# Optimization experiments

Measured on AMD Instinct MI355X. Metric: run time of the kernel, lower is better.

Reference implementation:

```python
import jax, jax.numpy as jnp
import numpy as np
import math

B, S, E, H = 2, 2048, 1024, 8
Dh = E // H  # 128


def setup_inputs() -> dict:
    key = jax.random.key(0)
    ks = jax.random.split(key, 9)
    g = lambda k, shp: jax.random.normal(k, shp, jnp.float32) * 0.02
    return {
        "inputs": jax.random.normal(ks[0], (B, S, E), jnp.float32),
        "ln_gamma": jnp.ones((E,), jnp.float32),
        "ln_beta": jnp.zeros((E,), jnp.float32),
        "Wq": g(ks[1], (Dh, Dh)), "bq": jnp.zeros((Dh,), jnp.float32),
        "Wk": g(ks[2], (Dh, Dh)), "bk": jnp.zeros((Dh,), jnp.float32),
        "Wv": g(ks[3], (Dh, Dh)), "bv": jnp.zeros((Dh,), jnp.float32),
        "Wp": g(ks[4], (Dh, Dh)),  # pos_proj has no bias
        "u_bias": g(ks[5], (H, Dh)),
        "v_bias": g(ks[6], (H, Dh)),
        "Wo": g(ks[7], (E, E)), "bo": jnp.zeros((E,), jnp.float32),
    }


def _pos_encoding(s, e):
    # sinusoidal PE, interleaved sin/cos as in the torch module
    pos = jnp.arange(s, dtype=jnp.float32)[:, None]
    div = jnp.exp(jnp.arange(0, e, 2, dtype=jnp.float32) * (-math.log(10000.0) / e))
    pe = jnp.zeros((s, e), jnp.float32)
    pe = pe.at[:, 0::2].set(jnp.sin(pos * div))
    pe = pe.at[:, 1::2].set(jnp.cos(pos * div))
    return pe


def _rel_shift(ps):
    # Transformer-XL relative shift: pad a zero column, reshape, drop first row
    b, h, s1, s2 = ps.shape
    padded = jnp.pad(ps, ((0, 0), (0, 0), (0, 0), (1, 0)))
    return padded.reshape(b, h, s2 + 1, s1)[:, :, 1:, :].reshape(b, h, s1, s2)


def _forward(inputs, ln_gamma, ln_beta, Wq, bq, Wk, bk, Wv, bv, Wp, u_bias, v_bias, Wo, bo):
    b, s, e = inputs.shape
    # LayerNorm (biased variance, eps=1e-5 like nn.LayerNorm)
    mu = inputs.mean(-1, keepdims=True)
    var = inputs.var(-1, keepdims=True)
    xn = (inputs - mu) / jnp.sqrt(var + 1e-5) * ln_gamma + ln_beta

    xh = xn.reshape(b, s, H, Dh)              # split heads before per-head Dh x Dh projections
    q = xh @ Wq + bq                           # (b, s, H, Dh)
    k = xh @ Wk + bk
    v = xh @ Wv + bv

    pe = _pos_encoding(s, e).reshape(s, H, Dh)  # same for every batch element
    p = pe @ Wp                                 # (s, H, Dh)

    content = jnp.einsum('bqhd,bkhd->bhqk', q + u_bias, k)
    pos_score = jnp.einsum('bqhd,khd->bhqk', q + v_bias, p)
    pos_score = _rel_shift(pos_score)
    score = (content + pos_score) / jnp.sqrt(jnp.float32(e))  # note: scales by sqrt(embed_dim), faithful to source

    attn = jax.nn.softmax(score, axis=-1)
    ctx = jnp.einsum('bhqk,bkhd->bqhd', attn, v).reshape(b, s, e)
    # dropout is identity at inference
    return ctx @ Wo + bo


def reference(inputs, ln_gamma, ln_beta, Wq, bq, Wk, bk, Wv, bv, Wp, u_bias, v_bias, Wo, bo):
    return _forward(inputs, ln_gamma, ln_beta, Wq, bq, Wk, bk, Wv, bv, Wp, u_bias, v_bias, Wo, bo)
```

## Files before the change

kernel.cpp:

```cpp
#include <hip/hip_runtime.h>
#include <hip/hip_bf16.h>

#define SDIM 2048
#define EDIM 1024

typedef __attribute__((ext_vector_type(8))) short bf16x8;
typedef __attribute__((ext_vector_type(4))) short bf16x4;
typedef __attribute__((ext_vector_type(4))) float f32x4;
typedef __hip_bfloat16 bf16;

#define MFMA(a, b, c) __builtin_amdgcn_mfma_f32_16x16x32_bf16((a), (b), (c), 0, 0, 0)

#define GLDS16(g, l)                                                      \
  __builtin_amdgcn_global_load_lds(                                       \
      (const __attribute__((address_space(1))) unsigned int*)(g),         \
      (__attribute__((address_space(3))) unsigned int*)(l), 16, 0, 0)

__device__ __forceinline__ bf16x8 ld8(const bf16* p) {
  return *(const bf16x8*)p;
}
__device__ __forceinline__ float b2f(short s) {
  union { float f; unsigned u; } v; v.u = ((unsigned)(unsigned short)s) << 16; return v.f;
}

__device__ __forceinline__ void wcast_body(const float* __restrict__ w, bf16* __restrict__ wt,
                                           int blk, int R, int C) {
  __shared__ float tile[32][33];
  int cb = C >> 5;
  int br = blk / cb, bc = blk % cb;
  int r0 = br << 5, c0 = bc << 5;
  int tr = threadIdx.x >> 5, tc = threadIdx.x & 31;
#pragma unroll
  for (int i = 0; i < 32; i += 8)
    tile[tr + i][tc] = w[(size_t)(r0 + tr + i) * C + c0 + tc];
  __syncthreads();
#pragma unroll
  for (int i = 0; i < 32; i += 8)
    wt[(size_t)(c0 + tr + i) * R + r0 + tc] = __float2bfloat16(tile[tc][tr + i]);
}

__global__ __launch_bounds__(256) void wcast_all(const float* __restrict__ wo, const float* __restrict__ w0,
                                                 const float* __restrict__ w1, const float* __restrict__ w2,
                                                 const float* __restrict__ w3, bf16* __restrict__ oo,
                                                 bf16* __restrict__ o0, bf16* __restrict__ o1,
                                                 bf16* __restrict__ o2, bf16* __restrict__ o3) {
  int blk = blockIdx.x;
  if (blk < 1024) {
    wcast_body(wo, oo, blk, 1024, 1024);
  } else {
    int which = (blk - 1024) >> 4;
    const float* w = which == 0 ? w0 : which == 1 ? w1 : which == 2 ? w2 : w3;
    bf16* o = which == 0 ? o0 : which == 1 ? o1 : which == 2 ? o2 : o3;
    wcast_body(w, o, (blk - 1024) & 15, 128, 128);
  }
}

__global__ __launch_bounds__(256) void ln_kernel(const float* __restrict__ x, const float* __restrict__ g,
                                                 const float* __restrict__ be, bf16* __restrict__ xn) {
  int tok = blockIdx.x;
  const float4 v = ((const float4*)(x + (size_t)tok * EDIM))[threadIdx.x];
  float s = v.x + v.y + v.z + v.w;
  float s2 = v.x * v.x + v.y * v.y + v.z * v.z + v.w * v.w;
#pragma unroll
  for (int o = 1; o < 64; o <<= 1) { s += __shfl_xor(s, o); s2 += __shfl_xor(s2, o); }
  __shared__ float ls[8];
  if ((threadIdx.x & 63) == 0) { ls[threadIdx.x >> 6] = s; ls[4 + (threadIdx.x >> 6)] = s2; }
  __syncthreads();
  s = ls[0] + ls[1] + ls[2] + ls[3];
  s2 = ls[4] + ls[5] + ls[6] + ls[7];
  float mu = s * (1.0f / EDIM);
  float rstd = rsqrtf(s2 * (1.0f / EDIM) - mu * mu + 1e-5f);
  int c = threadIdx.x * 4;
  const float4 gv = ((const float4*)g)[threadIdx.x];
  const float4 bv = ((const float4*)be)[threadIdx.x];
  bf16* o = xn + (size_t)tok * EDIM + c;
  o[0] = __float2bfloat16((v.x - mu) * rstd * gv.x + bv.x);
  o[1] = __float2bfloat16((v.y - mu) * rstd * gv.y + bv.y);
  o[2] = __float2bfloat16((v.z - mu) * rstd * gv.z + bv.z);
  o[3] = __float2bfloat16((v.w - mu) * rstd * gv.w + bv.w);
}

__global__ __launch_bounds__(256) void pe_kernel(bf16* __restrict__ pe) {
  int s = blockIdx.x;
  for (int i = threadIdx.x; i < EDIM / 2; i += 256) {
    float div = __expf((float)(2 * i) * (-9.210340371976184f / (float)EDIM));
    float a = (float)s * div;
    float sv, cv;
    sincosf(a, &sv, &cv);
    pe[(size_t)s * EDIM + 2 * i] = __float2bfloat16(sv);
    pe[(size_t)s * EDIM + 2 * i + 1] = __float2bfloat16(cv);
  }
}

template <int MODE>
__device__ __forceinline__ void proj_body(const bf16* __restrict__ A, const bf16* __restrict__ WT,
                                          const float* __restrict__ bias, const float* __restrict__ ubias,
                                          const float* __restrict__ vbias, bf16* __restrict__ out0,
                                          bf16* __restrict__ out1, int blk, bf16* tl) {
  const int row0 = blk * 128;
  const int lane = threadIdx.x & 63, wid = threadIdx.x >> 6;
  const int wr = (wid >> 1) * 64, wc = (wid & 1) * 64;
  const int lg = lane >> 4, lr = lane & 15;
  f32x4 acc[4][4] = {};
#pragma unroll
  for (int kf = 0; kf < 4; ++kf) {
    const int k0 = kf * 32 + lg * 8;
    bf16x8 a[4], b[4];
#pragma unroll
    for (int m = 0; m < 4; ++m) a[m] = ld8(A + (size_t)(row0 + wr + m * 16 + lr) * 128 + k0);
#pragma unroll
    for (int n = 0; n < 4; ++n) b[n] = ld8(WT + (size_t)(wc + n * 16 + lr) * 128 + k0);
#pragma unroll
    for (int m = 0; m < 4; ++m)
#pragma unroll
      for (int n = 0; n < 4; ++n) acc[m][n] = MFMA(a[m], b[n], acc[m][n]);
  }
  if constexpr (MODE == 2) {
#pragma unroll
    for (int m = 0; m < 4; ++m)
#pragma unroll
      for (int n = 0; n < 4; ++n) {
        int col = wc + n * 16 + lr;
#pragma unroll
        for (int r = 0; r < 4; ++r) {
          int lrow = wr + m * 16 + lg * 4 + r;
          tl[col * 132 + lrow] = __float2bfloat16(acc[m][n][r] + bias[col]);
        }
      }
    __syncthreads();
    int tok0 = row0 >> 3;
    int b = tok0 >> 11, s0 = tok0 & 2047;
#pragma unroll
    for (int i = 0; i < 4; ++i) {
      int pair = threadIdx.x + 256 * i;
      int h = pair >> 7, d = pair & 127;
      bf16 tmp[16];
#pragma unroll
      for (int j = 0; j < 16; ++j) tmp[j] = tl[d * 132 + j * 8 + h];
      size_t o = ((size_t)((b * 8 + h) * 128 + d)) * SDIM + s0;
      *(bf16x8*)(out0 + o) = *(bf16x8*)(&tmp[0]);
      *(bf16x8*)(out0 + o + 8) = *(bf16x8*)(&tmp[8]);
    }
  } else {
#pragma unroll
    for (int m = 0; m < 4; ++m)
#pragma unroll
      for (int n = 0; n < 4; ++n) {
        int col = wc + n * 16 + lr;
#pragma unroll
        for (int r = 0; r < 4; ++r) {
          int row = row0 + wr + m * 16 + lg * 4 + r;
          float val = acc[m][n][r];
          if constexpr (MODE == 0) {
            int h = row & 7, tok = row >> 3;
            int b = tok >> 11, s = tok & 2047;
            size_t o = ((size_t)((b * 8 + h) * SDIM + s)) * 128 + col;
            val += bias[col];
            out0[o] = __float2bfloat16((val + ubias[h * 128 + col]) * 0.03125f);
            out1[o] = __float2bfloat16((val + vbias[h * 128 + col]) * 0.03125f);
          } else if constexpr (MODE == 1) {
            int h = row & 7, tok = row >> 3;
            int b = tok >> 11, s = tok & 2047;
            out0[((size_t)((b * 8 + h) * SDIM + s)) * 128 + col] = __float2bfloat16(val + bias[col]);
          } else {
            int h = row & 7, s = row >> 3;
            out0[((size_t)(h * SDIM + s)) * 128 + col] = __float2bfloat16(val);
          }
        }
      }
  }
}

__global__ __launch_bounds__(256) void proj_all(const bf16* __restrict__ xn, const bf16* __restrict__ peb,
                                                const bf16* __restrict__ wqt, const bf16* __restrict__ wkt,
                                                const bf16* __restrict__ wvt, const bf16* __restrict__ wpt,
                                                const float* __restrict__ bq, const float* __restrict__ bk,
                                                const float* __restrict__ bv, const float* __restrict__ ub,
                                                const float* __restrict__ vbias, bf16* __restrict__ qub,
                                                bf16* __restrict__ qvb, bf16* __restrict__ kbb,
                                                bf16* __restrict__ vtb, bf16* __restrict__ pb) {
  __shared__ bf16 tl[128 * 132];
  int blk = blockIdx.x;
  if (blk < 256) proj_body<0>(xn, wqt, bq, ub, vbias, qub, qvb, blk, tl);
  else if (blk < 512) proj_body<1>(xn, wkt, bk, nullptr, nullptr, kbb, nullptr, blk - 256, tl);
  else if (blk < 768) proj_body<2>(xn, wvt, bv, nullptr, nullptr, vtb, nullptr, blk - 512, tl);
  else proj_body<3>(peb, wpt, nullptr, nullptr, nullptr, pb, nullptr, blk - 768, tl);
}

__global__ __launch_bounds__(256) void ps_kernel(const bf16* __restrict__ qv, const bf16* __restrict__ p,
                                                 bf16* __restrict__ ps) {
  const int bh = blockIdx.x & 15;
  const int t = blockIdx.x >> 4;
  const int q0 = (t >> 4) * 128, j0 = (t & 15) * 128;
  const int h = bh & 7;
  const bf16* Aq = qv + (size_t)bh * SDIM * 128;
  const bf16* Ph = p + (size_t)h * SDIM * 128;
  const int lane = threadIdx.x & 63, wid = threadIdx.x >> 6;
  const int wr = (wid >> 1) * 64, wc = (wid & 1) * 64;
  const int lg = lane >> 4, lr = lane & 15;
  f32x4 acc[4][4] = {};
#pragma unroll
  for (int kf = 0; kf < 4; ++kf) {
    const int k0 = kf * 32 + lg * 8;
    bf16x8 a[4], b[4];
#pragma unroll
    for (int m = 0; m < 4; ++m) a[m] = ld8(Aq + (size_t)(q0 + wr + m * 16 + lr) * 128 + k0);
#pragma unroll
    for (int n = 0; n < 4; ++n) b[n] = ld8(Ph + (size_t)(j0 + wc + n * 16 + lr) * 128 + k0);
#pragma unroll
    for (int m = 0; m < 4; ++m)
#pragma unroll
      for (int n = 0; n < 4; ++n) acc[m][n] = MFMA(a[m], b[n], acc[m][n]);
  }
  __shared__ bf16 tl[128 * 136];
#pragma unroll
  for (int m = 0; m < 4; ++m)
#pragma unroll
    for (int n = 0; n < 4; ++n) {
      int jl = wc + n * 16 + lr;
#pragma unroll
      for (int r = 0; r < 4; ++r) {
        int ql = wr + m * 16 + lg * 4 + r;
        tl[ql * 136 + jl] = __float2bfloat16(acc[m][n][r]);
      }
    }
  __syncthreads();
  bf16* po = ps + (size_t)bh * SDIM * SDIM + (size_t)q0 * SDIM + j0;
#pragma unroll
  for (int i = 0; i < 8; ++i) {
    int id = threadIdx.x + 256 * i;
    int row = id >> 4, seg = id & 15;
    bf16x8 v = *(const bf16x8*)(tl + row * 136 + seg * 8);
    *(bf16x8*)(po + (size_t)row * SDIM + seg * 8) = v;
  }
}

__global__ __launch_bounds__(512) void attn_kernel(const bf16* __restrict__ qu, const bf16* __restrict__ kb,
                                                   const bf16* __restrict__ vt, const bf16* __restrict__ ps,
                                                   bf16* __restrict__ ctx) {
  const int bh = blockIdx.x & 15, qblk = blockIdx.x >> 4;
  const int b = bh >> 3, h = bh & 7;
  const int lane = threadIdx.x & 63, wid = threadIdx.x >> 6;
  const int lg = lane >> 4, lr = lane & 15;
  const int q0 = qblk * 128 + wid * 16;
  const bf16* Kp = kb + (size_t)bh * SDIM * 128;
  const bf16* Vp = vt + (size_t)bh * 128 * SDIM;

  const bf16* psbh = ps + (size_t)bh * SDIM * SDIM;
  const int Q = q0 + lr;
  const bf16* pA = psbh + (size_t)(Q + 1) * (SDIM - 1);
  const bf16* pB = psbh + (size_t)(Q + 1) * SDIM - Q - 2;
  const int padA = (int)(((unsigned)(Q + 1) * (SDIM - 1)) & 3);
  const int padB = (int)(((unsigned)(Q + 1) * SDIM - Q - 2) & 3);

  __shared__ bf16 kl[2][64 * 128];
  __shared__ bf16 vl[2][128 * 64];
  __shared__ bf16 pl[8][16 * 72];
  bf16* plw = &pl[wid][0];

  const int krow_l = lane >> 4, kc16 = lane & 15;
  const int vrow_l = lane >> 3, vc8 = lane & 7;

  auto stageK = [&](int kt, int buf) {
#pragma unroll
    for (int i = 0; i < 2; ++i) {
      int rb = wid * 8 + i * 4;
      int row = rb + krow_l;
      GLDS16(Kp + (size_t)(kt + row) * 128 + ((kc16 ^ (row & 7)) << 3), &kl[buf][rb * 128]);
    }
  };
  auto stageV = [&](int kt, int buf) {
#pragma unroll
    for (int i = 0; i < 2; ++i) {
      int rb = wid * 16 + i * 8;
      int d = rb + vrow_l;
      GLDS16(Vp + (size_t)d * SDIM + kt + ((vc8 ^ (d & 7)) << 3), &vl[buf][rb * 64]);
    }
  };

  bf16x8 qfr[4];
#pragma unroll
  for (int kf = 0; kf < 4; ++kf)
    qfr[kf] = ld8(qu + (size_t)bh * SDIM * 128 + (size_t)(q0 + lr) * 128 + kf * 32 + lg * 8);

  f32x4 cacc[8] = {};
  float rsum = 0.f;

  unsigned long long wlo[4], whi[4];
  auto psload = [&](int kt) {
#pragma unroll
    for (int nf = 0; nf < 4; ++nf) {
      const int K0 = kt + nf * 16 + lg * 4;
      const bool a_ = (K0 + 3 <= Q);
      const bf16* wp = a_ ? (pA + K0 - padA) : (pB + K0 - padB);
      wlo[nf] = *(const unsigned long long*)wp;
      whi[nf] = *(const unsigned long long*)(wp + 4);
    }
  };
  psload(0);
  stageK(0, 0);
  stageV(0, 0);
  __syncthreads();

  int cur = 0;
  for (int kt = 0; kt < SDIM; kt += 64) {
    if (kt + 64 < SDIM) {
      stageK(kt + 64, cur ^ 1);
      stageV(kt + 64, cur ^ 1);
    }
    const bf16* klc = &kl[cur][0];
    const bf16* vlc = &vl[cur][0];
    f32x4 sc[4] = {};
#pragma unroll
    for (int nf = 0; nf < 4; ++nf) {
      const int krow = nf * 16 + lr;
      const bf16* kr = klc + krow * 128;
      const int sw = (krow & 7) << 3;
#pragma unroll
      for (int kf = 0; kf < 4; ++kf) {
        bf16x8 kfrag = *(const bf16x8*)(kr + (((kf * 4 + lg) << 3) ^ sw));
        sc[nf] = MFMA(kfrag, qfr[kf], sc[nf]);
      }
    }
    bf16x4 pscur[4];
#pragma unroll
    for (int nf = 0; nf < 4; ++nf) {
      const int K0 = kt + nf * 16 + lg * 4;
      const bool a_ = (K0 + 3 <= Q);
      const bool bp = (K0 >= Q + 2);
      const int sh = (a_ ? padA : padB) << 4;
      unsigned long long w = sh ? ((wlo[nf] >> sh) | (whi[nf] << (64 - sh))) : wlo[nf];
      union { unsigned long long u; bf16x4 v; } cv;
      cv.u = w;
      bf16x4 pv = cv.v;
      if (!a_ && !bp) {
#pragma unroll
        for (int r = 0; r < 4; ++r) {
          const int K = K0 + r;
          if (K <= Q) pv[r] = ((const short*)pA)[K];
          else if (K == Q + 1) pv[r] = (short)0;
        }
      }
      pscur[nf] = pv;
    }
    if (kt + 64 < SDIM) psload(kt + 64);
#pragma unroll
    for (int nf = 0; nf < 4; ++nf) {
      float e0 = __expf(sc[nf][0] + b2f(pscur[nf][0]));
      float e1 = __expf(sc[nf][1] + b2f(pscur[nf][1]));
      float e2 = __expf(sc[nf][2] + b2f(pscur[nf][2]));
      float e3 = __expf(sc[nf][3] + b2f(pscur[nf][3]));
      rsum += (e0 + e1) + (e2 + e3);
      bf16 tmp[4] = {__float2bfloat16(e0), __float2bfloat16(e1),
                     __float2bfloat16(e2), __float2bfloat16(e3)};
      *(bf16x4*)(plw + lr * 72 + nf * 16 + lg * 4) = *(bf16x4*)tmp;
    }
    bf16x8 pa[2];
#pragma unroll
    for (int k2 = 0; k2 < 2; ++k2)
      pa[k2] = *(const bf16x8*)(plw + lr * 72 + k2 * 32 + lg * 8);
#pragma unroll
    for (int nf = 0; nf < 8; ++nf) {
      const int d = nf * 16 + lr;
      const bf16* vr = vlc + d * 64;
      const int swd = (d & 7) << 3;
#pragma unroll
      for (int k2 = 0; k2 < 2; ++k2) {
        bf16x8 vb = *(const bf16x8*)(vr + (((k2 * 4 + lg) << 3) ^ swd));
        cacc[nf] = MFMA(pa[k2], vb, cacc[nf]);
      }
    }
    __syncthreads();
    cur ^= 1;
  }
  rsum += __shfl_xor(rsum, 16);
  rsum += __shfl_xor(rsum, 32);
  float inv[4];
#pragma unroll
  for (int r = 0; r < 4; ++r) inv[r] = 1.0f / __shfl(rsum, lg * 4 + r);
#pragma unroll
  for (int nf = 0; nf < 8; ++nf) {
#pragma unroll
    for (int r = 0; r < 4; ++r) {
      int q = q0 + lg * 4 + r;
      int d = nf * 16 + lr;
      ctx[((size_t)(b * SDIM + q) * 8 + h) * 128 + d] = __float2bfloat16(cacc[nf][r] * inv[r]);
    }
  }
}

__global__ __launch_bounds__(256) void out_gemm(const bf16* __restrict__ A, const bf16* __restrict__ WT,
                                                const float* __restrict__ bo, float* __restrict__ out) {
  const int bm = blockIdx.x >> 3, bn = blockIdx.x & 7;
  const int lane = threadIdx.x & 63, wid = threadIdx.x >> 6;
  const int wr = (wid >> 1) * 64, wc = (wid & 1) * 64;
  const int lg = lane >> 4, lr = lane & 15;
  const int row0 = bm * 128, col0 = bn * 128;
  f32x4 acc[4][4] = {};
  for (int kf = 0; kf < 32; ++kf) {
    const int k0 = kf * 32 + lg * 8;
    bf16x8 a[4], b[4];
#pragma unroll
    for (int m = 0; m < 4; ++m) a[m] = ld8(A + (size_t)(row0 + wr + m * 16 + lr) * 1024 + k0);
#pragma unroll
    for (int n = 0; n < 4; ++n) b[n] = ld8(WT + (size_t)(col0 + wc + n * 16 + lr) * 1024 + k0);
#pragma unroll
    for (int m = 0; m < 4; ++m)
#pragma unroll
      for (int n = 0; n < 4; ++n) acc[m][n] = MFMA(a[m], b[n], acc[m][n]);
  }
#pragma unroll
  for (int m = 0; m < 4; ++m)
#pragma unroll
    for (int n = 0; n < 4; ++n) {
      int col = col0 + wc + n * 16 + lr;
#pragma unroll
      for (int r = 0; r < 4; ++r) {
        int row = row0 + wr + m * 16 + lg * 4 + r;
        out[(size_t)row * 1024 + col] = acc[m][n][r] + bo[col];
      }
    }
}

extern "C" void kernel_launch(void* const* d_in, const int* in_sizes, int n_in,
                              void* d_out, int out_size, void* d_ws, size_t ws_size,
                              hipStream_t stream) {
  (void)in_sizes; (void)n_in; (void)out_size;
  const float* x = (const float*)d_in[0];
  const float* gam = (const float*)d_in[1];
  const float* bet = (const float*)d_in[2];
  const float* Wq = (const float*)d_in[3];
  const float* bq = (const float*)d_in[4];
  const float* Wk = (const float*)d_in[5];
  const float* bk = (const float*)d_in[6];
  const float* Wv = (const float*)d_in[7];
  const float* bv = (const float*)d_in[8];
  const float* Wp = (const float*)d_in[9];
  const float* ub = (const float*)d_in[10];
  const float* vbias = (const float*)d_in[11];
  const float* Wo = (const float*)d_in[12];
  const float* bo = (const float*)d_in[13];
  float* out = (float*)d_out;

  char* w = (char*)d_ws;
  size_t off = 0;
  auto take = [&](size_t n) { void* p = w + off; off += (n + 255) & ~(size_t)255; return p; };
  bf16* xn = (bf16*)take((size_t)4096 * 1024 * 2);
  bf16* peb = (bf16*)take((size_t)2048 * 1024 * 2);
  bf16* wqt = (bf16*)take(128 * 128 * 2);
  bf16* wkt = (bf16*)take(128 * 128 * 2);
  bf16* wvt = (bf16*)take(128 * 128 * 2);
  bf16* wpt = (bf16*)take(128 * 128 * 2);
  bf16* wot = (bf16*)take((size_t)1024 * 1024 * 2);
  bf16* qub = (bf16*)take((size_t)16 * 2048 * 128 * 2);
  bf16* qvb = (bf16*)take((size_t)16 * 2048 * 128 * 2);
  bf16* kbb = (bf16*)take((size_t)16 * 2048 * 128 * 2);
  bf16* vtb = (bf16*)take((size_t)16 * 2048 * 128 * 2);
  bf16* pb = (bf16*)take((size_t)8 * 2048 * 128 * 2);
  bf16* ctx = (bf16*)take((size_t)4096 * 1024 * 2);
  bf16* psb = (bf16*)take((size_t)16 * 2048 * 2048 * 2 + 4096);
  if (off > ws_size) return;

  wcast_all<<<1088, 256, 0, stream>>>(Wo, Wq, Wk, Wv, Wp, wot, wqt, wkt, wvt, wpt);
  ln_kernel<<<4096, 256, 0, stream>>>(x, gam, bet, xn);
  pe_kernel<<<2048, 256, 0, stream>>>(peb);
  proj_all<<<896, 256, 0, stream>>>(xn, peb, wqt, wkt, wvt, wpt, bq, bk, bv, ub, vbias,
                                    qub, qvb, kbb, vtb, pb);
  ps_kernel<<<4096, 256, 0, stream>>>(qvb, pb, psb);
  attn_kernel<<<256, 512, 0, stream>>>(qub, kbb, vtb, psb, ctx);
  out_gemm<<<256, 256, 0, stream>>>(ctx, wot, bo, out);
}
```

Measured before the change: 214.9 us.

## Retile attention to 64-query blocks with 32-key tiles and use raw exp2

```diff
diff --git a/kernel.cpp b/kernel.cpp
--- a/kernel.cpp
+++ b/kernel.cpp
@@ -21,6 +21,11 @@
 }
 __device__ __forceinline__ float b2f(short s) {
   union { float f; unsigned u; } v; v.u = ((unsigned)(unsigned short)s) << 16; return v.f;
+}
+__device__ __forceinline__ float fexp2(float x) {
+  float r;
+  asm("v_exp_f32 %0, %1" : "=v"(r) : "v"(x));
+  return r;
 }
 
 __device__ __forceinline__ void wcast_body(const float* __restrict__ w, bf16* __restrict__ wt,
@@ -92,6 +97,7 @@
   }
 }
 
+#define QSCALE 0.045084219879837156f
 template <int MODE>
 __device__ __forceinline__ void proj_body(const bf16* __restrict__ A, const bf16* __restrict__ WT,
                                           const float* __restrict__ bias, const float* __restrict__ ubias,
@@ -156,8 +162,8 @@
             int b = tok >> 11, s = tok & 2047;
             size_t o = ((size_t)((b * 8 + h) * SDIM + s)) * 128 + col;
             val += bias[col];
-            out0[o] = __float2bfloat16((val + ubias[h * 128 + col]) * 0.03125f);
-            out1[o] = __float2bfloat16((val + vbias[h * 128 + col]) * 0.03125f);
+            out0[o] = __float2bfloat16((val + ubias[h * 128 + col]) * QSCALE);
+            out1[o] = __float2bfloat16((val + vbias[h * 128 + col]) * QSCALE);
           } else if constexpr (MODE == 1) {
             int h = row & 7, tok = row >> 3;
             int b = tok >> 11, s = tok & 2047;
@@ -235,14 +241,14 @@
   }
 }
 
-__global__ __launch_bounds__(512) void attn_kernel(const bf16* __restrict__ qu, const bf16* __restrict__ kb,
-                                                   const bf16* __restrict__ vt, const bf16* __restrict__ ps,
-                                                   bf16* __restrict__ ctx) {
+__global__ __launch_bounds__(256, 4) void attn_kernel(const bf16* __restrict__ qu, const bf16* __restrict__ kb,
+                                                      const bf16* __restrict__ vt, const bf16* __restrict__ ps,
+                                                      bf16* __restrict__ ctx) {
   const int bh = blockIdx.x & 15, qblk = blockIdx.x >> 4;
   const int b = bh >> 3, h = bh & 7;
   const int lane = threadIdx.x & 63, wid = threadIdx.x >> 6;
   const int lg = lane >> 4, lr = lane & 15;
-  const int q0 = qblk * 128 + wid * 16;
+  const int q0 = qblk * 64 + wid * 16;
   const bf16* Kp = kb + (size_t)bh * SDIM * 128;
   const bf16* Vp = vt + (size_t)bh * 128 * SDIM;
 
@@ -253,13 +259,13 @@
   const int padA = (int)(((unsigned)(Q + 1) * (SDIM - 1)) & 3);
   const int padB = (int)(((unsigned)(Q + 1) * SDIM - Q - 2) & 3);
 
-  __shared__ bf16 kl[2][64 * 128];
-  __shared__ bf16 vl[2][128 * 64];
-  __shared__ bf16 pl[8][16 * 72];
+  __shared__ bf16 kl[2][32 * 128];
+  __shared__ bf16 vl[2][128 * 32];
+  __shared__ bf16 pl[4][16 * 40];
   bf16* plw = &pl[wid][0];
 
   const int krow_l = lane >> 4, kc16 = lane & 15;
-  const int vrow_l = lane >> 3, vc8 = lane & 7;
+  const int vrow_l = lane >> 2, vc4 = lane & 3;
 
   auto stageK = [&](int kt, int buf) {
 #pragma unroll
@@ -272,9 +278,9 @@
   auto stageV = [&](int kt, int buf) {
 #pragma unroll
     for (int i = 0; i < 2; ++i) {
-      int rb = wid * 16 + i * 8;
+      int rb = wid * 32 + i * 16;
       int d = rb + vrow_l;
-      GLDS16(Vp + (size_t)d * SDIM + kt + ((vc8 ^ (d & 7)) << 3), &vl[buf][rb * 64]);
+      GLDS16(Vp + (size_t)d * SDIM + kt + ((vc4 ^ (d & 3)) << 3), &vl[buf][rb * 32]);
     }
   };
 
@@ -286,10 +292,10 @@
   f32x4 cacc[8] = {};
   float rsum = 0.f;
 
-  unsigned long long wlo[4], whi[4];
+  unsigned long long wlo[2], whi[2];
   auto psload = [&](int kt) {
 #pragma unroll
-    for (int nf = 0; nf < 4; ++nf) {
+    for (int nf = 0; nf < 2; ++nf) {
       const int K0 = kt + nf * 16 + lg * 4;
       const bool a_ = (K0 + 3 <= Q);
       const bf16* wp = a_ ? (pA + K0 - padA) : (pB + K0 - padB);
@@ -303,16 +309,18 @@
   __syncthreads();
 
   int cur = 0;
-  for (int kt = 0; kt < SDIM; kt += 64) {
-    if (kt + 64 < SDIM) {
-      stageK(kt + 64, cur ^ 1);
-      stageV(kt + 64, cur ^ 1);
+  for (int t = 0; t < 64; ++t) {
+    const int kt = t * 32;
+    if (t < 63) {
+      stageK(kt + 32, cur ^ 1);
+      stageV(kt + 32, cur ^ 1);
     }
     const bf16* klc = &kl[cur][0];
     const bf16* vlc = &vl[cur][0];
-    f32x4 sc[4] = {};
-#pragma unroll
-    for (int nf = 0; nf < 4; ++nf) {
+    f32x4 sc[2] = {};
+    __builtin_amdgcn_s_setprio(1);
+#pragma unroll
+    for (int nf = 0; nf < 2; ++nf) {
       const int krow = nf * 16 + lr;
       const bf16* kr = klc + krow * 128;
       const int sw = (krow & 7) << 3;
@@ -322,9 +330,10 @@
         sc[nf] = MFMA(kfrag, qfr[kf], sc[nf]);
       }
     }
-    bf16x4 pscur[4];
-#pragma unroll
-    for (int nf = 0; nf < 4; ++nf) {
+    __builtin_amdgcn_s_setprio(0);
+    bf16x4 pscur[2];
+#pragma unroll
+    for (int nf = 0; nf < 2; ++nf) {
       const int K0 = kt + nf * 16 + lg * 4;
       const bool a_ = (K0 + 3 <= Q);
       const bool bp = (K0 >= Q + 2);
@@ -343,33 +352,28 @@
       }
       pscur[nf] = pv;
     }
-    if (kt + 64 < SDIM) psload(kt + 64);
-#pragma unroll
-    for (int nf = 0; nf < 4; ++nf) {
-      float e0 = __expf(sc[nf][0] + b2f(pscur[nf][0]));
-      float e1 = __expf(sc[nf][1] + b2f(pscur[nf][1]));
-      float e2 = __expf(sc[nf][2] + b2f(pscur[nf][2]));
-      float e3 = __expf(sc[nf][3] + b2f(pscur[nf][3]));
+    if (t < 63) psload(kt + 32);
+#pragma unroll
+    for (int nf = 0; nf < 2; ++nf) {
+      float e0 = fexp2(sc[nf][0] + b2f(pscur[nf][0]));
+      float e1 = fexp2(sc[nf][1] + b2f(pscur[nf][1]));
+      float e2 = fexp2(sc[nf][2] + b2f(pscur[nf][2]));
+      float e3 = fexp2(sc[nf][3] + b2f(pscur[nf][3]));
       rsum += (e0 + e1) + (e2 + e3);
       bf16 tmp[4] = {__float2bfloat16(e0), __float2bfloat16(e1),
                      __float2bfloat16(e2), __float2bfloat16(e3)};
-      *(bf16x4*)(plw + lr * 72 + nf * 16 + lg * 4) = *(bf16x4*)tmp;
-    }
-    bf16x8 pa[2];
-#pragma unroll
-    for (int k2 = 0; k2 < 2; ++k2)
-      pa[k2] = *(const bf16x8*)(plw + lr * 72 + k2 * 32 + lg * 8);
+      *(bf16x4*)(plw + lr * 40 + nf * 16 + lg * 4) = *(bf16x4*)tmp;
+    }
+    bf16x8 pa = *(const bf16x8*)(plw + lr * 40 + lg * 8);
+    __builtin_amdgcn_s_setprio(1);
 #pragma unroll
     for (int nf = 0; nf < 8; ++nf) {
       const int d = nf * 16 + lr;
-      const bf16* vr = vlc + d * 64;
-      const int swd = (d & 7) << 3;
-#pragma unroll
-      for (int k2 = 0; k2 < 2; ++k2) {
-        bf16x8 vb = *(const bf16x8*)(vr + (((k2 * 4 + lg) << 3) ^ swd));
-        cacc[nf] = MFMA(pa[k2], vb, cacc[nf]);
-      }
-    }
+      const bf16* vr = vlc + d * 32;
+      bf16x8 vb = *(const bf16x8*)(vr + (((lg ^ (d & 3))) << 3));
+      cacc[nf] = MFMA(pa, vb, cacc[nf]);
+    }
+    __builtin_amdgcn_s_setprio(0);
     __syncthreads();
     cur ^= 1;
   }
@@ -467,6 +471,6 @@
   proj_all<<<896, 256, 0, stream>>>(xn, peb, wqt, wkt, wvt, wpt, bq, bk, bv, ub, vbias,
                                     qub, qvb, kbb, vtb, pb);
   ps_kernel<<<4096, 256, 0, stream>>>(qvb, pb, psb);
-  attn_kernel<<<256, 512, 0, stream>>>(qub, kbb, vtb, psb, ctx);
+  attn_kernel<<<512, 256, 0, stream>>>(qub, kbb, vtb, psb, ctx);
   out_gemm<<<256, 256, 0, stream>>>(ctx, wot, bo, out);
 }
```

After: 220.2 us. 2.5% more time.
